# Optimization experiments

Measured on AMD Instinct MI355X. Metric: run time of the kernel, lower is better.

## Reference

```python
import jax, jax.numpy as jnp
from jax import lax
import numpy as np

# --- config (matches init_kwargs / cfgs.CLASS_NUM) ---
CLASS_NUM = 20
CONF_THRESH = 0.01
IOU_THRESH = 0.45
TOP_K = 200
NMS_MAX = 400
IMG_W = 300.0  # note: original code uses img_width for BOTH axes (bug replicated)
BATCH, N_BOXES = 64, 8732
LAST = 3 * CLASS_NUM + 5  # 65


def setup_inputs() -> dict:
    key = jax.random.key(0)
    y_pred = jax.random.uniform(key, (BATCH, N_BOXES, LAST), dtype=jnp.float32)
    return {"y_pred": y_pred}


def _iou_one_vs_many(box, boxes):
    # box: [4] (xmin,ymin,xmax,ymax); boxes: [M,4]
    x1 = jnp.maximum(box[0], boxes[:, 0])
    y1 = jnp.maximum(box[1], boxes[:, 1])
    x2 = jnp.minimum(box[2], boxes[:, 2])
    y2 = jnp.minimum(box[3], boxes[:, 3])
    inter = jnp.maximum(x2 - x1, 0.0) * jnp.maximum(y2 - y1, 0.0)
    area_a = jnp.maximum(box[2] - box[0], 0.0) * jnp.maximum(box[3] - box[1], 0.0)
    area_b = jnp.maximum(boxes[:, 2] - boxes[:, 0], 0.0) * jnp.maximum(boxes[:, 3] - boxes[:, 1], 0.0)
    union = area_a + area_b - inter
    return jnp.where(union > 0.0, inter / jnp.maximum(union, 1e-8), 0.0)


def _nms_item(preds):
    # preds: [N, 6] rows = [class_id, conf, xmin, ymin, xmax, ymax]
    conf = preds[:, 1]
    valid = conf > CONF_THRESH  # confidence thresholding (class_id != -1 is always true)
    # sort: valid boxes first, by descending confidence
    order = jnp.argsort(jnp.where(valid, -conf, jnp.inf))
    sp = preds[order]            # [N,6]
    sv = valid[order]            # [N]

    def step(state, inp):
        sel_pred, sel_mask, count = state  # [M,6], [M] float, int32
        p, v = inp
        ious = _iou_one_vs_many(p[2:6], sel_pred[:, 2:6]) * sel_mask
        keep = v & (count < NMS_MAX) & (jnp.max(ious) <= IOU_THRESH)
        w = jnp.minimum(count, NMS_MAX - 1)
        new_row = jnp.where(keep, p, sel_pred[w])
        sel_pred = sel_pred.at[w].set(new_row)
        sel_mask = sel_mask.at[w].set(jnp.where(keep, 1.0, sel_mask[w]))
        count = count + keep.astype(jnp.int32)
        return (sel_pred, sel_mask, count), None

    init = (jnp.zeros((NMS_MAX, 6), jnp.float32), jnp.zeros((NMS_MAX,), jnp.float32), jnp.int32(0))
    (sel_pred, sel_mask, _), _ = lax.scan(step, init, (sp, sv))
    sel_pred = sel_pred * sel_mask[:, None]  # zero-pad unselected slots
    # top_k by confidence, sorted descending (NMS_MAX >= TOP_K so always enough rows)
    _, top_idx = lax.top_k(sel_pred[:, 1], TOP_K)
    return sel_pred[top_idx]  # [TOP_K, 6]


def _forward(y_pred):
    C = CLASS_NUM
    # clip boxes to image boundary; original buggily uses img_width for both axes
    coords = jnp.clip(y_pred[..., -4:], 0.0, IMG_W - 1.0)  # [B,N,4] xmin,ymin,xmax,ymax
    probs = y_pred[..., C:2 * C] * y_pred[..., 2 * C + 1:-4]  # [B,N,C]
    class_ids = (jnp.argmax(probs, axis=-1) + 1).astype(jnp.float32)[..., None]
    confidences = jnp.max(probs, axis=-1, keepdims=True)
    preds = jnp.concatenate([class_ids, confidences, coords], axis=-1)  # [B,N,6]
    return jax.vmap(_nms_item)(preds)  # [B, TOP_K, 6]


def reference(y_pred):
    return _forward(y_pred)
```

## Files before the change

kernel.cpp:

```cpp
#include <hip/hip_runtime.h>
#include <cstdint>
#include <cstddef>

using u64 = unsigned long long;

namespace {
constexpr int kClassNum = 20;
constexpr int kBatch    = 64;
constexpr int kNBoxes   = 8732;
constexpr int kLast     = 65;
constexpr int kTopK     = 200;
constexpr int kNmsCap   = 200;
constexpr int kRows     = 128;
constexpr int kRBlocks  = (kNBoxes + kRows - 1) / kRows;
constexpr int kHist     = 1024;
constexpr int kSelM     = 512;
constexpr int kCand     = 1024;
constexpr int kFThreads = 1024;
constexpr int kConfThreads = 256;
constexpr int kNIter    = (kNBoxes + kFThreads - 1) / kFThreads;
constexpr int kGroups   = kCand / 64;
}

__device__ __forceinline__ int bucket_of(float c) {
  int b = (int)(__float_as_uint(c) >> 16) - 0x3C23;
  return min(max(b, 0), kHist - 1);
}

__device__ __forceinline__ float iou_f(float a0, float a1, float a2, float a3,
                                       float areaA, float4 bb) {
  const float ix1 = fmaxf(a0, bb.x);
  const float iy1 = fmaxf(a1, bb.y);
  const float ix2 = fminf(a2, bb.z);
  const float iy2 = fminf(a3, bb.w);
  const float inter = fmaxf(ix2 - ix1, 0.0f) * fmaxf(iy2 - iy1, 0.0f);
  const float areaB = fmaxf(bb.z - bb.x, 0.0f) * fmaxf(bb.w - bb.y, 0.0f);
  const float un = areaA + areaB - inter;
  return (un > 0.0f) ? inter / fmaxf(un, 1e-8f) : 0.0f;
}

__device__ __forceinline__ u64 readlane64(u64 x, int l) {
  const unsigned lo = (unsigned)__builtin_amdgcn_readlane((int)(unsigned)x, l);
  const unsigned hi = (unsigned)__builtin_amdgcn_readlane((int)(unsigned)(x >> 32), l);
  return ((u64)hi << 32) | (u64)lo;
}

__global__ __launch_bounds__(kConfThreads) void conf_kernel(const float* __restrict__ y,
                                                            float* __restrict__ confs) {
  __shared__ float tile[kRows * kLast];
  const int item = blockIdx.y;
  const int base = blockIdx.x * kRows;
  const int nb   = min(kRows, kNBoxes - base);
  const int tid  = threadIdx.x;

  const float4* src4 = (const float4*)(y + ((size_t)item * kNBoxes + base) * kLast);
  float4* t4 = (float4*)tile;
  const int nf4 = nb * kLast / 4;
  for (int k = tid; k < nf4; k += kConfThreads) t4[k] = src4[k];
  __syncthreads();

  if (tid < nb) {
    const float* row = tile + tid * kLast;
    float best = row[20] * row[41];
#pragma unroll
    for (int c = 1; c < kClassNum; ++c) best = fmaxf(best, row[20 + c] * row[41 + c]);
    confs[(size_t)item * kNBoxes + base + tid] = best;
  }
}

__device__ __forceinline__ u64 shfl_xor_u64(u64 x, int d) {
  int lo = __shfl_xor((int)(unsigned)x, d, 64);
  int hi = __shfl_xor((int)(unsigned)(x >> 32), d, 64);
  return ((u64)(unsigned)hi << 32) | (u64)(unsigned)lo;
}

__device__ __forceinline__ u64 cmpsel(u64 a, u64 b, bool keepmax) {
  u64 mx = a > b ? a : b;
  u64 mn = a > b ? b : a;
  return keepmax ? mx : mn;
}

template <int J, int K>
__device__ __forceinline__ void stage1(u64& k, int i, u64* buf) {
  if constexpr (J >= 64) {
    __syncthreads();
    buf[i] = k;
    __syncthreads();
    const u64 pv = buf[i ^ J];
    const bool lower = (i & J) == 0;
    const bool desc  = (i & K) == 0;
    k = cmpsel(k, pv, desc == lower);
  } else {
    const u64 pv = shfl_xor_u64(k, J);
    const bool lower = (i & J) == 0;
    const bool desc  = (i & K) == 0;
    k = cmpsel(k, pv, desc == lower);
  }
}

template <int K, int J>
__device__ __forceinline__ void cascade1(u64& k, int i, u64* buf) {
  stage1<J, K>(k, i, buf);
  if constexpr (J > 1) cascade1<K, (J >> 1)>(k, i, buf);
}

__global__ __launch_bounds__(kFThreads) void fused_kernel(const float* __restrict__ y,
                                                          const float* __restrict__ confs,
                                                          float* __restrict__ out) {
  __shared__ u64    buf[kCand];
  __shared__ int    hist[kHist];
  __shared__ int    wtot[16];
  __shared__ int    tails[16];
  __shared__ float4 selbox[kNmsCap];
  __shared__ float2 selmeta[kNmsCap];
  __shared__ float4 selact[kNmsCap];
  __shared__ float4 candbox[2][64];
  __shared__ float  candcls[2][64];
  __shared__ float  candconf[2][64];
  __shared__ u64    g_validm[2];
  __shared__ u64    supB[16];
  __shared__ u64    colm[64];
  __shared__ int g_thr, g_cnt, g_count, g_active, g_done;

  const int item = blockIdx.x;
  const int tid  = threadIdx.x;
  const int lane = tid & 63;
  const int wv   = tid >> 6;
  const float* cbase = confs + (size_t)item * kNBoxes;
  const float* ybase = y + (size_t)item * kNBoxes * kLast;

  hist[tid] = 0;
  if (tid == 0) { g_thr = 0; g_cnt = 0; g_count = 0; g_active = 0; g_done = 0; }
  __syncthreads();

  float cv[kNIter];
#pragma unroll
  for (int r = 0; r < kNIter; ++r) {
    const int i = tid + r * kFThreads;
    cv[r] = (i < kNBoxes) ? cbase[i] : 0.0f;
    if (cv[r] > 0.01f) atomicAdd(&hist[bucket_of(cv[r])], 1);
  }
  __syncthreads();

  {
    int v = hist[tid];
#pragma unroll
    for (int off = 1; off < 64; off <<= 1) {
      const int o = __shfl_down(v, off, 64);
      if (lane + off < 64) v += o;
    }
    if (lane == 0) wtot[wv] = v;
    __syncthreads();
    if (tid < 16) {
      int t = wtot[tid];
#pragma unroll
      for (int off = 1; off < 16; off <<= 1) {
        const int o = __shfl_down(t, off, 64);
        if (tid + off < 16) t += o;
      }
      tails[tid] = t - wtot[tid];
    }
    __syncthreads();
    hist[tid] = v + tails[wv];
  }
  __syncthreads();

  {
    const int S  = hist[tid];
    const int Sn = (tid < kHist - 1) ? hist[tid + 1] : 0;
    if (S >= kSelM && Sn < kSelM) g_thr = tid;
  }
  __syncthreads();
  const int T = g_thr;

#pragma unroll
  for (int r = 0; r < kNIter; ++r) {
    const int i = tid + r * kFThreads;
    const bool take = (i < kNBoxes) && (cv[r] > 0.01f) && (bucket_of(cv[r]) >= T);
    const u64 bal = __ballot(take);
    int wbase = 0;
    if (lane == 0 && bal) wbase = atomicAdd(&g_cnt, __popcll(bal));
    wbase = __shfl(wbase, 0, 64);
    if (take) {
      const int pos = wbase + __popcll(bal & ((1ull << lane) - 1ull));
      if (pos < kCand)
        buf[pos] = ((u64)__float_as_uint(cv[r]) << 32) |
                   (u64)(0xFFFFFFFFu - (unsigned)i);
    }
  }
  __syncthreads();
  const int ncand = min(g_cnt, kCand);
  for (int i2 = ncand + tid; i2 < kCand; i2 += kFThreads) buf[i2] = 0;
  __syncthreads();

  {
    u64 k = buf[tid];
    cascade1<2, 1>(k, tid, buf);
    cascade1<4, 2>(k, tid, buf);
    cascade1<8, 4>(k, tid, buf);
    cascade1<16, 8>(k, tid, buf);
    cascade1<32, 16>(k, tid, buf);
    cascade1<64, 32>(k, tid, buf);
    cascade1<128, 64>(k, tid, buf);
    cascade1<256, 128>(k, tid, buf);
    cascade1<512, 256>(k, tid, buf);
    cascade1<1024, 512>(k, tid, buf);
    __syncthreads();
    buf[tid] = k;
  }
  __syncthreads();

  auto gather = [&](int g, int slot) {
    float4 box = make_float4(0.f, 0.f, 0.f, 0.f);
    float cls = 0.f, cf = 0.f;
    int val = 0;
    if (g < kGroups) {
      const u64 key = buf[g * 64 + lane];
      if (key >> 32) {
        val = 1;
        cf = __uint_as_float((unsigned)(key >> 32));
        const unsigned idx = 0xFFFFFFFFu - (unsigned)key;
        const float* row = ybase + (size_t)idx * kLast;
        float best = row[20] * row[41];
        int cl = 1;
#pragma unroll
        for (int c = 1; c < kClassNum; ++c) {
          const float p = row[20 + c] * row[41 + c];
          if (p > best) { best = p; cl = c + 1; }
        }
        cls = (float)cl;
        const float c0 = fminf(fmaxf(row[61], 0.0f), 299.0f);
        const float c1 = fminf(fmaxf(row[62], 0.0f), 299.0f);
        const float c2 = fminf(fmaxf(row[63], 0.0f), 299.0f);
        const float c3 = fminf(fmaxf(row[64], 0.0f), 299.0f);
        box = make_float4(c0, c1, c2, c3);
      }
    }
    candbox[slot][lane]  = box;
    candcls[slot][lane]  = cls;
    candconf[slot][lane] = cf;
    const u64 vm = __ballot(val);
    if (lane == 0) g_validm[slot] = vm;
  };

  if (wv == 0) gather(0, 0);
  __syncthreads();

  int cur = 0;
  for (int g = 0; g < kGroups; ++g) {
    const int count = g_count;
    const int act   = g_active;

    const float4 bx = candbox[cur][lane];
    const float a0 = bx.x, a1 = bx.y, a2 = bx.z, a3 = bx.w;
    const float areaA = fmaxf(a2 - a0, 0.0f) * fmaxf(a3 - a1, 0.0f);
    float m = 0.0f;
    if (areaA > 0.0f) {
      for (int s = wv; s < act; s += 16) m = fmaxf(m, iou_f(a0, a1, a2, a3, areaA, selact[s]));
    }
    {
      const u64 pb = __ballot(m > 0.45f);
      if (lane == 0) supB[wv] = pb;
    }

#pragma unroll
    for (int jj = 0; jj < 4; ++jj) {
      const int j = wv * 4 + jj;
      const float4 bb = candbox[cur][j];
      const float areaB = fmaxf(bb.z - bb.x, 0.0f) * fmaxf(bb.w - bb.y, 0.0f);
      u64 cm = 0ull;
      if (areaB > 0.0f) {
        const float iou = iou_f(a0, a1, a2, a3, areaA, bb);
        cm = __ballot((j < lane) && (iou > 0.45f));
      }
      if (lane == 0) colm[j] = cm;
    }
    __syncthreads();

    if (wv == 1) gather(g + 1, cur ^ 1);
    if (wv == 0) {
      u64 supm = 0ull;
#pragma unroll
      for (int ww = 0; ww < 16; ++ww) supm |= supB[ww];
      const u64 mycol  = colm[lane];
      const u64 validm = g_validm[cur];

      u64 avail = validm & ~supm;
      u64 keptm = 0ull;
      int cnt  = count;
      int done = 0;
      while (avail) {
        const int j = __builtin_ctzll(avail);
        keptm |= (1ull << j);
        if (++cnt >= kNmsCap) { done = 1; break; }
        const u64 cj = readlane64(mycol, j);
        avail &= ~(cj | (1ull << j));
      }
      if (validm != ~0ull) done = 1;

      const u64 below = (1ull << lane) - 1ull;
      const u64 actm = keptm & __ballot(areaA > 0.0f);
      if ((keptm >> lane) & 1ull) {
        const int wdx = count + __popcll(keptm & below);
        if (wdx < kNmsCap) {
          selbox[wdx]  = bx;
          selmeta[wdx] = make_float2(candcls[cur][lane], candconf[cur][lane]);
        }
      }
      if ((actm >> lane) & 1ull) {
        const int adx = act + __popcll(actm & below);
        if (adx < kNmsCap) selact[adx] = bx;
      }
      if (lane == 0) {
        g_count  = min(cnt, kNmsCap);
        g_active = min(act + __popcll(actm), kNmsCap);
        g_done   = done;
      }
    }
    __syncthreads();
    if (g_done) break;
    cur ^= 1;
  }

  const int count = g_count;
  float* obase = out + (size_t)item * kTopK * 6;
  for (int slot = tid; slot < kTopK; slot += kFThreads) {
    float* o = obase + (size_t)slot * 6;
    if (slot < count) {
      const float4 bsel = selbox[slot];
      const float2 mta  = selmeta[slot];
      o[0] = mta.x; o[1] = mta.y; o[2] = bsel.x; o[3] = bsel.y; o[4] = bsel.z; o[5] = bsel.w;
    } else {
      o[0] = 0.0f; o[1] = 0.0f; o[2] = 0.0f; o[3] = 0.0f; o[4] = 0.0f; o[5] = 0.0f;
    }
  }
}

extern "C" void kernel_launch(void* const* d_in, const int* in_sizes, int n_in,
                              void* d_out, int out_size, void* d_ws, size_t ws_size,
                              hipStream_t stream) {
  const float* y = (const float*)d_in[0];
  float* out = (float*)d_out;

  float* confs = (float*)d_ws;

  dim3 cgrid(kRBlocks, kBatch);
  conf_kernel<<<cgrid, kConfThreads, 0, stream>>>(y, confs);
  fused_kernel<<<kBatch, kFThreads, 0, stream>>>(y, confs, out);
}
```

Baseline: 71.06 us.

## Prefilter high-confidence candidates into a global pool and shrink the sort to 512

The conf kernel now reads each row straight from global memory instead of staging it in LDS. It also appends boxes whose confidence exceeds 0.9 to a per-item pool through warp-ballot atomics. The fused kernel loads this small pool when it holds enough entries, and falls back to the full confidence scan otherwise. The candidate count and the bitonic sort shrink from 1024 to 512, with the selection threshold bucket adjusted so the candidates fit. This is meant to cut global reads and sort work in the fused kernel, at the cost of an extra memset, global atomics, and uncoalesced row reads in the conf kernel.

```diff
diff --git a/kernel.cpp b/kernel.cpp
--- a/kernel.cpp
+++ b/kernel.cpp
@@ -11,19 +11,21 @@
 constexpr int kLast     = 65;
 constexpr int kTopK     = 200;
 constexpr int kNmsCap   = 200;
-constexpr int kRows     = 128;
-constexpr int kRBlocks  = (kNBoxes + kRows - 1) / kRows;
 constexpr int kHist     = 1024;
-constexpr int kSelM     = 512;
-constexpr int kCand     = 1024;
+constexpr int kSelM     = 384;
+constexpr int kCand     = 512;
+constexpr int kPool     = 2048;
+constexpr float kPreT   = 0.9f;
 constexpr int kFThreads = 1024;
 constexpr int kConfThreads = 256;
+constexpr int kCBlocks  = (kNBoxes + kConfThreads - 1) / kConfThreads;
 constexpr int kNIter    = (kNBoxes + kFThreads - 1) / kFThreads;
+constexpr int kPoolIter = kPool / kFThreads;
 constexpr int kGroups   = kCand / 64;
 }
 
-__device__ __forceinline__ int bucket_of(float c) {
-  int b = (int)(__float_as_uint(c) >> 16) - 0x3C23;
+__device__ __forceinline__ int bucket_of_key(u64 k) {
+  int b = (int)(unsigned)(k >> 48) - 0x3C23;
   return min(max(b, 0), kHist - 1);
 }
 
@@ -46,25 +48,43 @@
 }
 
 __global__ __launch_bounds__(kConfThreads) void conf_kernel(const float* __restrict__ y,
-                                                            float* __restrict__ confs) {
-  __shared__ float tile[kRows * kLast];
+                                                            float* __restrict__ confs,
+                                                            u64* __restrict__ pool,
+                                                            int* __restrict__ gcnt) {
   const int item = blockIdx.y;
-  const int base = blockIdx.x * kRows;
-  const int nb   = min(kRows, kNBoxes - base);
-  const int tid  = threadIdx.x;
-
-  const float4* src4 = (const float4*)(y + ((size_t)item * kNBoxes + base) * kLast);
-  float4* t4 = (float4*)tile;
-  const int nf4 = nb * kLast / 4;
-  for (int k = tid; k < nf4; k += kConfThreads) t4[k] = src4[k];
-  __syncthreads();
-
-  if (tid < nb) {
-    const float* row = tile + tid * kLast;
-    float best = row[20] * row[41];
-#pragma unroll
-    for (int c = 1; c < kClassNum; ++c) best = fmaxf(best, row[20 + c] * row[41 + c]);
-    confs[(size_t)item * kNBoxes + base + tid] = best;
+  const int r    = blockIdx.x * kConfThreads + threadIdx.x;
+  const int lane = threadIdx.x & 63;
+
+  float conf = 0.0f;
+  if (r < kNBoxes) {
+    const float* row = y + ((size_t)item * kNBoxes + r) * kLast;
+    float a[40];
+#pragma unroll
+    for (int q = 0; q < 10; ++q) {
+      const float4 v = *(const float4*)(row + 20 + 4 * q);
+      a[4 * q + 0] = v.x; a[4 * q + 1] = v.y; a[4 * q + 2] = v.z; a[4 * q + 3] = v.w;
+    }
+    const float s60 = row[60];
+    float best = a[0] * a[21];
+#pragma unroll
+    for (int c = 1; c < kClassNum; ++c) {
+      const float w = (c < 19) ? a[21 + c] : s60;
+      best = fmaxf(best, a[c] * w);
+    }
+    conf = best;
+    confs[(size_t)item * kNBoxes + r] = best;
+  }
+
+  const bool take = conf > kPreT;
+  const u64 bal = __ballot(take);
+  int wbase = 0;
+  if (lane == 0 && bal) wbase = atomicAdd(&gcnt[item], __popcll(bal));
+  wbase = __shfl(wbase, 0, 64);
+  if (take) {
+    const int pos = wbase + __popcll(bal & ((1ull << lane) - 1ull));
+    if (pos < kPool)
+      pool[(size_t)item * kPool + pos] =
+          ((u64)__float_as_uint(conf) << 32) | (u64)(0xFFFFFFFFu - (unsigned)r);
   }
 }
 
@@ -81,15 +101,17 @@
 }
 
 template <int J, int K>
-__device__ __forceinline__ void stage1(u64& k, int i, u64* buf) {
+__device__ __forceinline__ void stage1(u64& k, int i, bool act, u64* buf) {
   if constexpr (J >= 64) {
     __syncthreads();
-    buf[i] = k;
-    __syncthreads();
-    const u64 pv = buf[i ^ J];
-    const bool lower = (i & J) == 0;
-    const bool desc  = (i & K) == 0;
-    k = cmpsel(k, pv, desc == lower);
+    if (act) buf[i] = k;
+    __syncthreads();
+    if (act) {
+      const u64 pv = buf[i ^ J];
+      const bool lower = (i & J) == 0;
+      const bool desc  = (i & K) == 0;
+      k = cmpsel(k, pv, desc == lower);
+    }
   } else {
     const u64 pv = shfl_xor_u64(k, J);
     const bool lower = (i & J) == 0;
@@ -99,13 +121,15 @@
 }
 
 template <int K, int J>
-__device__ __forceinline__ void cascade1(u64& k, int i, u64* buf) {
-  stage1<J, K>(k, i, buf);
-  if constexpr (J > 1) cascade1<K, (J >> 1)>(k, i, buf);
+__device__ __forceinline__ void cascade1(u64& k, int i, bool act, u64* buf) {
+  stage1<J, K>(k, i, act, buf);
+  if constexpr (J > 1) cascade1<K, (J >> 1)>(k, i, act, buf);
 }
 
 __global__ __launch_bounds__(kFThreads) void fused_kernel(const float* __restrict__ y,
                                                           const float* __restrict__ confs,
+                                                          const u64* __restrict__ pool,
+                                                          const int* __restrict__ gcnt,
                                                           float* __restrict__ out) {
   __shared__ u64    buf[kCand];
   __shared__ int    hist[kHist];
@@ -120,26 +144,43 @@
   __shared__ u64    g_validm[2];
   __shared__ u64    supB[16];
   __shared__ u64    colm[64];
-  __shared__ int g_thr, g_cnt, g_count, g_active, g_done;
+  __shared__ int g_cnt, g_count, g_active, g_done, g_thr;
 
   const int item = blockIdx.x;
   const int tid  = threadIdx.x;
   const int lane = tid & 63;
   const int wv   = tid >> 6;
   const float* cbase = confs + (size_t)item * kNBoxes;
+  const u64* pbase = pool + (size_t)item * kPool;
   const float* ybase = y + (size_t)item * kNBoxes * kLast;
 
   hist[tid] = 0;
-  if (tid == 0) { g_thr = 0; g_cnt = 0; g_count = 0; g_active = 0; g_done = 0; }
-  __syncthreads();
-
-  float cv[kNIter];
-#pragma unroll
-  for (int r = 0; r < kNIter; ++r) {
-    const int i = tid + r * kFThreads;
-    cv[r] = (i < kNBoxes) ? cbase[i] : 0.0f;
-    if (cv[r] > 0.01f) atomicAdd(&hist[bucket_of(cv[r])], 1);
-  }
+  if (tid == 0) { g_cnt = 0; g_count = 0; g_active = 0; g_done = 0; g_thr = 0; }
+
+  const int pcnt = gcnt[item];
+  const bool usePool = (pcnt >= kSelM) && (pcnt <= kPool);
+  u64 kv[kNIter];
+  if (usePool) {
+#pragma unroll
+    for (int r = 0; r < kNIter; ++r) {
+      const int i = tid + r * kFThreads;
+      kv[r] = (r < kPoolIter && i < pcnt) ? pbase[i] : 0ull;
+    }
+  } else {
+#pragma unroll
+    for (int r = 0; r < kNIter; ++r) {
+      const int i = tid + r * kFThreads;
+      const float c = (i < kNBoxes) ? cbase[i] : 0.0f;
+      kv[r] = (c > 0.01f)
+                  ? (((u64)__float_as_uint(c) << 32) | (u64)(0xFFFFFFFFu - (unsigned)i))
+                  : 0ull;
+    }
+  }
+  __syncthreads();
+
+#pragma unroll
+  for (int r = 0; r < kNIter; ++r)
+    if (kv[r]) atomicAdd(&hist[bucket_of_key(kv[r])], 1);
   __syncthreads();
 
   {
@@ -171,21 +212,19 @@
     if (S >= kSelM && Sn < kSelM) g_thr = tid;
   }
   __syncthreads();
-  const int T = g_thr;
+  const int T0 = g_thr;
+  const int T  = (hist[T0] > kCand && T0 < kHist - 1) ? T0 + 1 : T0;
 
 #pragma unroll
   for (int r = 0; r < kNIter; ++r) {
-    const int i = tid + r * kFThreads;
-    const bool take = (i < kNBoxes) && (cv[r] > 0.01f) && (bucket_of(cv[r]) >= T);
+    const bool take = kv[r] && (bucket_of_key(kv[r]) >= T);
     const u64 bal = __ballot(take);
     int wbase = 0;
     if (lane == 0 && bal) wbase = atomicAdd(&g_cnt, __popcll(bal));
     wbase = __shfl(wbase, 0, 64);
     if (take) {
       const int pos = wbase + __popcll(bal & ((1ull << lane) - 1ull));
-      if (pos < kCand)
-        buf[pos] = ((u64)__float_as_uint(cv[r]) << 32) |
-                   (u64)(0xFFFFFFFFu - (unsigned)i);
+      if (pos < kCand) buf[pos] = kv[r];
     }
   }
   __syncthreads();
@@ -194,19 +233,19 @@
   __syncthreads();
 
   {
-    u64 k = buf[tid];
-    cascade1<2, 1>(k, tid, buf);
-    cascade1<4, 2>(k, tid, buf);
-    cascade1<8, 4>(k, tid, buf);
-    cascade1<16, 8>(k, tid, buf);
-    cascade1<32, 16>(k, tid, buf);
-    cascade1<64, 32>(k, tid, buf);
-    cascade1<128, 64>(k, tid, buf);
-    cascade1<256, 128>(k, tid, buf);
-    cascade1<512, 256>(k, tid, buf);
-    cascade1<1024, 512>(k, tid, buf);
-    __syncthreads();
-    buf[tid] = k;
+    const bool act = tid < kCand;
+    u64 k = act ? buf[tid] : 0ull;
+    cascade1<2, 1>(k, tid, act, buf);
+    cascade1<4, 2>(k, tid, act, buf);
+    cascade1<8, 4>(k, tid, act, buf);
+    cascade1<16, 8>(k, tid, act, buf);
+    cascade1<32, 16>(k, tid, act, buf);
+    cascade1<64, 32>(k, tid, act, buf);
+    cascade1<128, 64>(k, tid, act, buf);
+    cascade1<256, 128>(k, tid, act, buf);
+    cascade1<512, 256>(k, tid, act, buf);
+    __syncthreads();
+    if (act) buf[tid] = k;
   }
   __syncthreads();
 
@@ -287,12 +326,12 @@
 
       u64 avail = validm & ~supm;
       u64 keptm = 0ull;
-      int cnt  = count;
+      int cnt2 = count;
       int done = 0;
       while (avail) {
         const int j = __builtin_ctzll(avail);
         keptm |= (1ull << j);
-        if (++cnt >= kNmsCap) { done = 1; break; }
+        if (++cnt2 >= kNmsCap) { done = 1; break; }
         const u64 cj = readlane64(mycol, j);
         avail &= ~(cj | (1ull << j));
       }
@@ -312,7 +351,7 @@
         if (adx < kNmsCap) selact[adx] = bx;
       }
       if (lane == 0) {
-        g_count  = min(cnt, kNmsCap);
+        g_count  = min(cnt2, kNmsCap);
         g_active = min(act + __popcll(actm), kNmsCap);
         g_done   = done;
       }
@@ -343,8 +382,11 @@
   float* out = (float*)d_out;
 
   float* confs = (float*)d_ws;
-
-  dim3 cgrid(kRBlocks, kBatch);
-  conf_kernel<<<cgrid, kConfThreads, 0, stream>>>(y, confs);
-  fused_kernel<<<kBatch, kFThreads, 0, stream>>>(y, confs, out);
-}
+  u64* pool = (u64*)(confs + (size_t)kBatch * kNBoxes);
+  int* gcnt = (int*)(pool + (size_t)kBatch * kPool);
+
+  hipMemsetAsync(gcnt, 0, kBatch * sizeof(int), stream);
+  dim3 cgrid(kCBlocks, kBatch);
+  conf_kernel<<<cgrid, kConfThreads, 0, stream>>>(y, confs, pool, gcnt);
+  fused_kernel<<<kBatch, kFThreads, 0, stream>>>(y, confs, pool, gcnt, out);
+}
```

New measurement: 131.6 us. 85.2% more time.
